# Kernel optimization log

Measured on AMD Instinct MI355X. Metric: run time of the kernel, lower is better.

The kernel has to match this reference:

```python
import jax, jax.numpy as jnp
import numpy as np

N_NODES = 100000
N_EDGES = 1600000
N_FEAT = 64
HIDDEN = 64
OUT = 1
NUM_GRAPHS = 256
N_STACK_LAYERS = 4  # layers 0..3 are 64->64->64; layer 4 is 64->1->1


def setup_inputs() -> dict:
    key = jax.random.key(0)
    ks = jax.random.split(key, 12)
    x = jax.random.normal(ks[0], (N_NODES, N_FEAT), dtype=jnp.float32)
    edge_index = jax.random.randint(ks[1], (2, N_EDGES), 0, N_NODES, dtype=jnp.int64)
    batch = jnp.sort(jax.random.randint(ks[2], (N_NODES,), 0, NUM_GRAPHS, dtype=jnp.int64))
    s = 1.0 / np.sqrt(HIDDEN)
    # Stacked params for the 4 identical (64->64->64) GIN MLPs
    W1 = jax.random.uniform(ks[3], (N_STACK_LAYERS, HIDDEN, HIDDEN), jnp.float32, -s, s)
    b1 = jax.random.uniform(ks[4], (N_STACK_LAYERS, HIDDEN), jnp.float32, -s, s)
    W2 = jax.random.uniform(ks[5], (N_STACK_LAYERS, HIDDEN, HIDDEN), jnp.float32, -s, s)
    b2 = jax.random.uniform(ks[6], (N_STACK_LAYERS, HIDDEN), jnp.float32, -s, s)
    # Last layer MLP: [64 -> 1 -> 1]
    W1_last = jax.random.uniform(ks[7], (HIDDEN, OUT), jnp.float32, -s, s)
    b1_last = jax.random.uniform(ks[8], (OUT,), jnp.float32, -s, s)
    W2_last = jax.random.uniform(ks[9], (OUT, OUT), jnp.float32, -1.0, 1.0)
    b2_last = jax.random.uniform(ks[10], (OUT,), jnp.float32, -1.0, 1.0)
    return {"x": x, "edge_index": edge_index, "batch": batch,
            "W1": W1, "b1": b1, "W2": W2, "b2": b2,
            "W1_last": W1_last, "b1_last": b1_last,
            "W2_last": W2_last, "b2_last": b2_last}


def _gin_conv(x, src, dst, w1, bb1, w2, bb2):
    # GINConv: mlp((1+eps)*x + sum_{j in N(i)} x_j), eps=0
    agg = jax.ops.segment_sum(x[src], dst, num_segments=N_NODES)
    h = agg + x
    h = jnp.maximum(h @ w1 + bb1, 0.0)  # Linear + ReLU inside MLP
    return h @ w2 + bb2                 # plain last Linear of MLP


def reference(x, edge_index, batch, W1, b1, W2, b2, W1_last, b1_last, W2_last, b2_last):
    src, dst = edge_index[0], edge_index[1]  # message: x[src] -> dst (source_to_target)
    h = x
    for i in range(N_STACK_LAYERS):
        h = _gin_conv(h, src, dst, W1[i], b1[i], W2[i], b2[i])
        h = jnp.maximum(h, 0.0)  # inter-layer ReLU (dropout = identity in eval)
    h = _gin_conv(h, src, dst, W1_last, b1_last, W2_last, b2_last)  # last layer: no act
    # global mean pool over graphs
    sums = jax.ops.segment_sum(h, batch, num_segments=NUM_GRAPHS)
    counts = jax.ops.segment_sum(jnp.ones((N_NODES, 1), dtype=h.dtype), batch,
                                 num_segments=NUM_GRAPHS)
    return sums / jnp.maximum(counts, 1.0)
```

## Files before the change

kernel.cpp:

```cpp
#include <hip/hip_runtime.h>
#include <hip/hip_bf16.h>

#define N_NODES 100000
#define N_EDGES 1600000
#define FEAT 64
#define NGRAPH 256

#define SCAN_CHUNK 1024
#define SCAN_BLOCKS ((N_NODES + SCAN_CHUNK - 1) / SCAN_CHUNK)

#define CB_SHIFT 10
#define CB_NODES 1024
#define NCB ((N_NODES + CB_NODES - 1) / CB_NODES)
#define CB_CAP 18432

#define PB 512
#define EPB ((N_EDGES + PB - 1) / PB)

#define NTILES (N_NODES / 16)
#define MLP_BLOCKS 1024

typedef unsigned short u16;
typedef unsigned int u32;
typedef __attribute__((ext_vector_type(8))) short short8;
typedef __attribute__((ext_vector_type(4))) float f32x4;

static __device__ __forceinline__ float bf2f(u16 h) {
    return __uint_as_float(((u32)h) << 16);
}
static __device__ __forceinline__ u16 f2bf(float x) {
    u32 u = __float_as_uint(x);
    return (u16)((u + 0x7FFF + ((u >> 16) & 1)) >> 16);
}
static __device__ __forceinline__ float2 up2(u32 v) {
    return make_float2(bf2f((u16)(v & 0xFFFF)), bf2f((u16)(v >> 16)));
}
static __device__ __forceinline__ short8 as_short8(uint4 v) {
    union { uint4 u; short8 s; } c; c.u = v; return c.s;
}


__global__ __launch_bounds__(256) void k_phist(const int* __restrict__ dst,
                                               int* __restrict__ bhist) {
    __shared__ int cnt[NCB];
    int t = threadIdx.x;
    for (int i = t; i < NCB; i += 256) cnt[i] = 0;
    __syncthreads();
    int begin = blockIdx.x * EPB;
    int end = begin + EPB; if (end > N_EDGES) end = N_EDGES;
    for (int e = begin + t; e < end; e += 256)
        atomicAdd(&cnt[dst[e] >> CB_SHIFT], 1);
    __syncthreads();
    for (int i = t; i < NCB; i += 256) bhist[i * PB + blockIdx.x] = cnt[i];
}

__global__ __launch_bounds__(PB) void k_pscan(int* __restrict__ bhist,
                                              int* __restrict__ gtot) {
    __shared__ int s[PB];
    int b = blockIdx.x, t = threadIdx.x;
    int v = bhist[b * PB + t];
    s[t] = v;
    __syncthreads();
    for (int off = 1; off < PB; off <<= 1) {
        int add = (t >= off) ? s[t - off] : 0;
        __syncthreads();
        s[t] += add;
        __syncthreads();
    }
    int incl = s[t];
    bhist[b * PB + t] = (t ? s[t - 1] : 0);
    if (t == PB - 1) gtot[b] = incl;
}

__global__ __launch_bounds__(256) void k_pscatter(const int* __restrict__ src,
                                                  const int* __restrict__ dst,
                                                  const int* __restrict__ bhist,
                                                  int* __restrict__ tmp) {
    __shared__ int cur[NCB];
    int t = threadIdx.x;
    for (int i = t; i < NCB; i += 256) cur[i] = bhist[i * PB + blockIdx.x];
    __syncthreads();
    int begin = blockIdx.x * EPB;
    int end = begin + EPB; if (end > N_EDGES) end = N_EDGES;
    for (int e = begin + t; e < end; e += 256) {
        int d = dst[e];
        int b = d >> CB_SHIFT;
        int pos = atomicAdd(&cur[b], 1);
        if (pos < CB_CAP) tmp[b * CB_CAP + pos] = ((d & (CB_NODES - 1)) << 17) | src[e];
    }
}


__global__ __launch_bounds__(256) void k_bdeg(const int* __restrict__ tmp,
                                              const int* __restrict__ gtot,
                                              int* __restrict__ deg) {
    __shared__ int cnt[CB_NODES];
    int b = blockIdx.x, t = threadIdx.x;
    for (int j = t; j < CB_NODES; j += 256) cnt[j] = 0;
    __syncthreads();
    int n = gtot[b]; if (n > CB_CAP) n = CB_CAP;
    const int* tp = &tmp[b * CB_CAP];
    for (int i = t; i < n; i += 256) atomicAdd(&cnt[tp[i] >> 17], 1);
    __syncthreads();
    int n0 = b << CB_SHIFT;
    for (int j = t; j < CB_NODES; j += 256) {
        int node = n0 + j;
        if (node < N_NODES) deg[node] = cnt[j];
    }
}


__global__ __launch_bounds__(256) void k_scan1(const int* __restrict__ deg,
                                               int* __restrict__ bsum) {
    int t = threadIdx.x;
    int base = blockIdx.x * SCAN_CHUNK + t * 4;
    int4 d = make_int4(0, 0, 0, 0);
    if (base + 3 < N_NODES) {
        d = *reinterpret_cast<const int4*>(&deg[base]);
    } else {
        if (base + 0 < N_NODES) d.x = deg[base + 0];
        if (base + 1 < N_NODES) d.y = deg[base + 1];
        if (base + 2 < N_NODES) d.z = deg[base + 2];
    }
    int v = d.x + d.y + d.z + d.w;
#pragma unroll
    for (int off = 32; off; off >>= 1) v += __shfl_xor(v, off);
    __shared__ int red[4];
    int lane = t & 63, wid = t >> 6;
    if (lane == 0) red[wid] = v;
    __syncthreads();
    if (t == 0) bsum[blockIdx.x] = red[0] + red[1] + red[2] + red[3];
}

__global__ __launch_bounds__(128) void k_scan2(int* __restrict__ bsum) {
    __shared__ int s[128];
    int t = threadIdx.x;
    int v = (t < SCAN_BLOCKS) ? bsum[t] : 0;
    s[t] = v;
    __syncthreads();
    for (int off = 1; off < 128; off <<= 1) {
        int add = (t >= off) ? s[t - off] : 0;
        __syncthreads();
        s[t] += add;
        __syncthreads();
    }
    if (t < SCAN_BLOCKS) bsum[t] = (t ? s[t - 1] : 0);
}

__global__ __launch_bounds__(256) void k_scan3(int* __restrict__ deg_off,
                                               const int* __restrict__ bsum) {
    int t = threadIdx.x;
    int base = blockIdx.x * SCAN_CHUNK + t * 4;
    int4 d = make_int4(0, 0, 0, 0);
    bool full = (base + 3 < N_NODES);
    if (full) {
        d = *reinterpret_cast<const int4*>(&deg_off[base]);
    } else {
        if (base + 0 < N_NODES) d.x = deg_off[base + 0];
        if (base + 1 < N_NODES) d.y = deg_off[base + 1];
        if (base + 2 < N_NODES) d.z = deg_off[base + 2];
    }
    int total = d.x + d.y + d.z + d.w;
    __shared__ int sc[256];
    sc[t] = total;
    __syncthreads();
    for (int off = 1; off < 256; off <<= 1) {
        int add = (t >= off) ? sc[t - off] : 0;
        __syncthreads();
        sc[t] += add;
        __syncthreads();
    }
    int texc = (t ? sc[t - 1] : 0) + bsum[blockIdx.x];
    int4 o;
    o.x = texc;
    o.y = o.x + d.x;
    o.z = o.y + d.y;
    o.w = o.z + d.z;
    if (full) {
        *reinterpret_cast<int4*>(&deg_off[base]) = o;
    } else {
        if (base + 0 < N_NODES) deg_off[base + 0] = o.x;
        if (base + 1 < N_NODES) deg_off[base + 1] = o.y;
        if (base + 2 < N_NODES) deg_off[base + 2] = o.z;
    }
}


__global__ __launch_bounds__(256) void k_bsort(const int* __restrict__ tmp,
                                               const int* __restrict__ offs,
                                               const int* __restrict__ gtot,
                                               int* __restrict__ ssrc) {
    __shared__ int lcur[CB_NODES];
    int b = blockIdx.x;
    int n0 = b << CB_SHIFT;
    int t = threadIdx.x;
    for (int j = t; j < CB_NODES; j += 256) {
        int n = n0 + j;
        lcur[j] = (n < N_NODES) ? offs[n] : 0;
    }
    __syncthreads();
    int cnt = gtot[b]; if (cnt > CB_CAP) cnt = CB_CAP;
    const int* tp = &tmp[b * CB_CAP];
    for (int i = t; i < cnt; i += 256) {
        int p = tp[i];
        int pos = atomicAdd(&lcur[p >> 17], 1);
        ssrc[pos] = p & 0x1FFFF;
    }
}


__global__ __launch_bounds__(256) void k_cvt(const float* __restrict__ x,
                                             u16* __restrict__ hb) {
    int i = blockIdx.x * 256 + threadIdx.x;
    const int total = N_NODES * FEAT / 8;
    if (i < total) {
        const float4* xv = (const float4*)x;
        float4 a = xv[2 * i], b = xv[2 * i + 1];
        uint4 o;
        o.x = f2bf(a.x) | ((u32)f2bf(a.y) << 16);
        o.y = f2bf(a.z) | ((u32)f2bf(a.w) << 16);
        o.z = f2bf(b.x) | ((u32)f2bf(b.y) << 16);
        o.w = f2bf(b.z) | ((u32)f2bf(b.w) << 16);
        ((uint4*)hb)[i] = o;
    }
}


__global__ __launch_bounds__(256) void k_aggregate(const u16* __restrict__ hb,
                                                   u32* __restrict__ aggb,
                                                   const int* __restrict__ offs,
                                                   const int* __restrict__ ssrc) {
    int grp = threadIdx.x >> 4;
    int li = threadIdx.x & 15;
    int node = blockIdx.x * 16 + grp;
    if (node >= N_NODES) return;
    const uint2* hb2 = (const uint2*)hb;
    uint2 pv = hb2[(size_t)node * 16 + li];
    float2 pa = up2(pv.x), pb = up2(pv.y);
    float v0 = pa.x, v1 = pa.y, v2 = pb.x, v3 = pb.y;
    int s = offs[node];
    int e = (node + 1 < N_NODES) ? offs[node + 1] : N_EDGES;
    int j = s;
    for (; j + 7 < e; j += 8) {
        int s0 = ssrc[j], s1 = ssrc[j + 1], s2 = ssrc[j + 2], s3 = ssrc[j + 3];
        int s4 = ssrc[j + 4], s5 = ssrc[j + 5], s6 = ssrc[j + 6], s7 = ssrc[j + 7];
        uint2 n0 = hb2[(size_t)s0 * 16 + li];
        uint2 n1 = hb2[(size_t)s1 * 16 + li];
        uint2 n2 = hb2[(size_t)s2 * 16 + li];
        uint2 n3 = hb2[(size_t)s3 * 16 + li];
        uint2 n4 = hb2[(size_t)s4 * 16 + li];
        uint2 n5 = hb2[(size_t)s5 * 16 + li];
        uint2 n6 = hb2[(size_t)s6 * 16 + li];
        uint2 n7 = hb2[(size_t)s7 * 16 + li];
        float2 a0 = up2(n0.x), b0 = up2(n0.y), a1 = up2(n1.x), b1 = up2(n1.y);
        float2 a2 = up2(n2.x), b2 = up2(n2.y), a3 = up2(n3.x), b3 = up2(n3.y);
        float2 a4 = up2(n4.x), b4 = up2(n4.y), a5 = up2(n5.x), b5 = up2(n5.y);
        float2 a6 = up2(n6.x), b6 = up2(n6.y), a7 = up2(n7.x), b7 = up2(n7.y);
        v0 += a0.x + a1.x + a2.x + a3.x + a4.x + a5.x + a6.x + a7.x;
        v1 += a0.y + a1.y + a2.y + a3.y + a4.y + a5.y + a6.y + a7.y;
        v2 += b0.x + b1.x + b2.x + b3.x + b4.x + b5.x + b6.x + b7.x;
        v3 += b0.y + b1.y + b2.y + b3.y + b4.y + b5.y + b6.y + b7.y;
    }
    if (j + 3 < e) {
        int s0 = ssrc[j], s1 = ssrc[j + 1], s2 = ssrc[j + 2], s3 = ssrc[j + 3];
        uint2 n0 = hb2[(size_t)s0 * 16 + li];
        uint2 n1 = hb2[(size_t)s1 * 16 + li];
        uint2 n2 = hb2[(size_t)s2 * 16 + li];
        uint2 n3 = hb2[(size_t)s3 * 16 + li];
        float2 a0 = up2(n0.x), b0 = up2(n0.y), a1 = up2(n1.x), b1 = up2(n1.y);
        float2 a2 = up2(n2.x), b2 = up2(n2.y), a3 = up2(n3.x), b3 = up2(n3.y);
        v0 += a0.x + a1.x + a2.x + a3.x;
        v1 += a0.y + a1.y + a2.y + a3.y;
        v2 += b0.x + b1.x + b2.x + b3.x;
        v3 += b0.y + b1.y + b2.y + b3.y;
        j += 4;
    }
    for (; j < e; ++j) {
        uint2 nv = hb2[(size_t)ssrc[j] * 16 + li];
        float2 a = up2(nv.x), b = up2(nv.y);
        v0 += a.x; v1 += a.y; v2 += b.x; v3 += b.y;
    }
    uint2 o;
    o.x = f2bf(v0) | ((u32)f2bf(v1) << 16);
    o.y = f2bf(v2) | ((u32)f2bf(v3) << 16);
    ((uint2*)aggb)[(size_t)node * 16 + li] = o;
}


__global__ __launch_bounds__(256) void k_mlp(const u32* __restrict__ aggb,
                                             u32* __restrict__ hout32,
                                             const float* __restrict__ W1,
                                             const float* __restrict__ b1,
                                             const float* __restrict__ W2,
                                             const float* __restrict__ b2) {
    __shared__ __align__(16) u32 lds[4 * 2 * 576];
    int wid = threadIdx.x >> 6;
    int lane = threadIdx.x & 63;
    int m = lane & 15;
    int g = lane >> 4;
    u32* H = &lds[wid * 2 * 576];
    u32* O = H + 576;

    short8 A1[4][2], A2[4][2];
    float bv1[4][4], bv2[4][4];
#pragma unroll
    for (int nt = 0; nt < 4; ++nt) {
        int n = nt * 16 + m;
#pragma unroll
        for (int kh = 0; kh < 2; ++kh) {
            short8 s1, s2;
#pragma unroll
            for (int j = 0; j < 8; ++j) {
                int k = kh * 32 + g * 8 + j;
                s1[j] = (short)f2bf(W1[k * 64 + n]);
                s2[j] = (short)f2bf(W2[k * 64 + n]);
            }
            A1[nt][kh] = s1;
            A2[nt][kh] = s2;
        }
#pragma unroll
        for (int r = 0; r < 4; ++r) {
            bv1[nt][r] = b1[nt * 16 + g * 4 + r];
            bv2[nt][r] = b2[nt * 16 + g * 4 + r];
        }
    }

    int gwave = blockIdx.x * 4 + wid;
    int nwaves = gridDim.x * 4;
    for (int tile = gwave; tile < NTILES; tile += nwaves) {
        int nodeBase = tile * 16;
        const uint4* bp = (const uint4*)(aggb + (size_t)(nodeBase + m) * 32);
        short8 B0 = as_short8(bp[g]);
        short8 B1f = as_short8(bp[4 + g]);

#pragma unroll
        for (int nt = 0; nt < 4; ++nt) {
            f32x4 acc = { bv1[nt][0], bv1[nt][1], bv1[nt][2], bv1[nt][3] };
            acc = __builtin_amdgcn_mfma_f32_16x16x32_bf16(A1[nt][0], B0, acc, 0, 0, 0);
            acc = __builtin_amdgcn_mfma_f32_16x16x32_bf16(A1[nt][1], B1f, acc, 0, 0, 0);
            float h0 = fmaxf(acc[0], 0.0f), h1 = fmaxf(acc[1], 0.0f);
            float h2 = fmaxf(acc[2], 0.0f), h3 = fmaxf(acc[3], 0.0f);
            H[m * 36 + nt * 8 + g * 2 + 0] = f2bf(h0) | ((u32)f2bf(h1) << 16);
            H[m * 36 + nt * 8 + g * 2 + 1] = f2bf(h2) | ((u32)f2bf(h3) << 16);
        }
        const uint4* hp = (const uint4*)H;
        short8 HB0 = as_short8(hp[9 * m + g]);
        short8 HB1 = as_short8(hp[9 * m + g + 4]);

#pragma unroll
        for (int nt = 0; nt < 4; ++nt) {
            f32x4 acc = { bv2[nt][0], bv2[nt][1], bv2[nt][2], bv2[nt][3] };
            acc = __builtin_amdgcn_mfma_f32_16x16x32_bf16(A2[nt][0], HB0, acc, 0, 0, 0);
            acc = __builtin_amdgcn_mfma_f32_16x16x32_bf16(A2[nt][1], HB1, acc, 0, 0, 0);
            float o0 = fmaxf(acc[0], 0.0f), o1 = fmaxf(acc[1], 0.0f);
            float o2 = fmaxf(acc[2], 0.0f), o3 = fmaxf(acc[3], 0.0f);
            O[m * 36 + nt * 8 + g * 2 + 0] = f2bf(o0) | ((u32)f2bf(o1) << 16);
            O[m * 36 + nt * 8 + g * 2 + 1] = f2bf(o2) | ((u32)f2bf(o3) << 16);
        }
        int m2 = lane >> 2;
        int q = (lane & 3) * 8;
        const uint4* op = (const uint4*)O;
        uint4 w0 = op[(m2 * 36 + q) >> 2];
        uint4 w1 = op[(m2 * 36 + q + 4) >> 2];
        uint4* gp = (uint4*)(hout32 + (size_t)(nodeBase + m2) * 32 + q);
        gp[0] = w0;
        gp[1] = w1;
    }
}


__global__ __launch_bounds__(256) void k_lastagg(const u16* __restrict__ hb,
                                                 const int* __restrict__ offs,
                                                 const int* __restrict__ ssrc,
                                                 const float* __restrict__ W1l,
                                                 const float* __restrict__ b1l,
                                                 const float* __restrict__ W2l,
                                                 const float* __restrict__ b2l,
                                                 float* __restrict__ o) {
    int grp = threadIdx.x >> 4;
    int li = threadIdx.x & 15;
    int node = blockIdx.x * 16 + grp;
    if (node >= N_NODES) return;
    const uint2* hb2 = (const uint2*)hb;
    uint2 pv = hb2[(size_t)node * 16 + li];
    float2 pa = up2(pv.x), pb = up2(pv.y);
    float v0 = pa.x, v1 = pa.y, v2 = pb.x, v3 = pb.y;
    int s = offs[node];
    int e = (node + 1 < N_NODES) ? offs[node + 1] : N_EDGES;
    int j = s;
    for (; j + 7 < e; j += 8) {
        int s0 = ssrc[j], s1 = ssrc[j + 1], s2 = ssrc[j + 2], s3 = ssrc[j + 3];
        int s4 = ssrc[j + 4], s5 = ssrc[j + 5], s6 = ssrc[j + 6], s7 = ssrc[j + 7];
        uint2 n0 = hb2[(size_t)s0 * 16 + li];
        uint2 n1 = hb2[(size_t)s1 * 16 + li];
        uint2 n2 = hb2[(size_t)s2 * 16 + li];
        uint2 n3 = hb2[(size_t)s3 * 16 + li];
        uint2 n4 = hb2[(size_t)s4 * 16 + li];
        uint2 n5 = hb2[(size_t)s5 * 16 + li];
        uint2 n6 = hb2[(size_t)s6 * 16 + li];
        uint2 n7 = hb2[(size_t)s7 * 16 + li];
        float2 a0 = up2(n0.x), b0 = up2(n0.y), a1 = up2(n1.x), b1 = up2(n1.y);
        float2 a2 = up2(n2.x), b2 = up2(n2.y), a3 = up2(n3.x), b3 = up2(n3.y);
        float2 a4 = up2(n4.x), b4 = up2(n4.y), a5 = up2(n5.x), b5 = up2(n5.y);
        float2 a6 = up2(n6.x), b6 = up2(n6.y), a7 = up2(n7.x), b7 = up2(n7.y);
        v0 += a0.x + a1.x + a2.x + a3.x + a4.x + a5.x + a6.x + a7.x;
        v1 += a0.y + a1.y + a2.y + a3.y + a4.y + a5.y + a6.y + a7.y;
        v2 += b0.x + b1.x + b2.x + b3.x + b4.x + b5.x + b6.x + b7.x;
        v3 += b0.y + b1.y + b2.y + b3.y + b4.y + b5.y + b6.y + b7.y;
    }
    if (j + 3 < e) {
        int s0 = ssrc[j], s1 = ssrc[j + 1], s2 = ssrc[j + 2], s3 = ssrc[j + 3];
        uint2 n0 = hb2[(size_t)s0 * 16 + li];
        uint2 n1 = hb2[(size_t)s1 * 16 + li];
        uint2 n2 = hb2[(size_t)s2 * 16 + li];
        uint2 n3 = hb2[(size_t)s3 * 16 + li];
        float2 a0 = up2(n0.x), b0 = up2(n0.y), a1 = up2(n1.x), b1 = up2(n1.y);
        float2 a2 = up2(n2.x), b2 = up2(n2.y), a3 = up2(n3.x), b3 = up2(n3.y);
        v0 += a0.x + a1.x + a2.x + a3.x;
        v1 += a0.y + a1.y + a2.y + a3.y;
        v2 += b0.x + b1.x + b2.x + b3.x;
        v3 += b0.y + b1.y + b2.y + b3.y;
        j += 4;
    }
    for (; j < e; ++j) {
        uint2 nv = hb2[(size_t)ssrc[j] * 16 + li];
        float2 a = up2(nv.x), b = up2(nv.y);
        v0 += a.x; v1 += a.y; v2 += b.x; v3 += b.y;
    }
    float4 wv = ((const float4*)W1l)[li];
    float v = v0 * wv.x + v1 * wv.y + v2 * wv.z + v3 * wv.w;
#pragma unroll
    for (int off = 8; off; off >>= 1) v += __shfl_xor(v, off);
    if (li == 0) {
        float h1 = fmaxf(v + b1l[0], 0.0f);
        o[node] = fmaf(h1, W2l[0], b2l[0]);
    }
}


__global__ __launch_bounds__(256) void k_pool(const float* __restrict__ o,
                                              const int* __restrict__ batch,
                                              float* __restrict__ out) {
    int g = blockIdx.x;
    int lo = 0, hi = N_NODES;
    while (lo < hi) { int mid = (lo + hi) >> 1; if (batch[mid] < g) lo = mid + 1; else hi = mid; }
    int start = lo;
    hi = N_NODES;
    while (lo < hi) { int mid = (lo + hi) >> 1; if (batch[mid] < g + 1) lo = mid + 1; else hi = mid; }
    int end = lo;

    float s = 0.0f;
    for (int i = start + threadIdx.x; i < end; i += 256) s += o[i];
#pragma unroll
    for (int off = 32; off; off >>= 1) s += __shfl_xor(s, off);
    __shared__ float red[4];
    int lane = threadIdx.x & 63, wid = threadIdx.x >> 6;
    if (lane == 0) red[wid] = s;
    __syncthreads();
    if (threadIdx.x == 0) {
        float t = red[0] + red[1] + red[2] + red[3];
        float c = (float)(end - start);
        out[g] = t / fmaxf(c, 1.0f);
    }
}


extern "C" void kernel_launch(void* const* d_in, const int* in_sizes, int n_in,
                              void* d_out, int out_size, void* d_ws, size_t ws_size,
                              hipStream_t stream) {
    const float* x    = (const float*)d_in[0];
    const int*   ei   = (const int*)d_in[1];
    const int*   bat  = (const int*)d_in[2];
    const float* W1   = (const float*)d_in[3];
    const float* b1   = (const float*)d_in[4];
    const float* W2   = (const float*)d_in[5];
    const float* b2   = (const float*)d_in[6];
    const float* W1l  = (const float*)d_in[7];
    const float* b1l  = (const float*)d_in[8];
    const float* W2l  = (const float*)d_in[9];
    const float* b2l  = (const float*)d_in[10];
    float* out = (float*)d_out;

    const int* srcI = ei;
    const int* dstI = ei + N_EDGES;

    char* ws = (char*)d_ws;
    u32*   aggb  = (u32*)ws;                                ws += (size_t)N_NODES * 32 * 4;
    u16*   hb    = (u16*)ws;                                ws += (size_t)N_NODES * FEAT * 2;
    int*   offs  = (int*)ws;                                ws += (size_t)N_NODES * 4;
    int*   ssrc  = (int*)ws;                                ws += (size_t)N_EDGES * 4;
    int*   tmp   = (int*)ws;                                ws += (size_t)NCB * CB_CAP * 4;
    float* onode = (float*)ws;                              ws += (size_t)N_NODES * 4;
    int*   bsum  = (int*)ws;                                ws += 128 * 4;
    int*   bhist = (int*)ws;                                ws += (size_t)NCB * PB * 4;
    int*   gtot  = (int*)ws;                                ws += ((NCB + 3) & ~3) * 4;

    k_phist<<<PB, 256, 0, stream>>>(dstI, bhist);
    k_pscan<<<NCB, PB, 0, stream>>>(bhist, gtot);
    k_pscatter<<<PB, 256, 0, stream>>>(srcI, dstI, bhist, tmp);
    k_bdeg<<<NCB, 256, 0, stream>>>(tmp, gtot, offs);
    k_scan1<<<SCAN_BLOCKS, 256, 0, stream>>>(offs, bsum);
    k_scan2<<<1, 128, 0, stream>>>(bsum);
    k_scan3<<<SCAN_BLOCKS, 256, 0, stream>>>(offs, bsum);
    k_bsort<<<NCB, 256, 0, stream>>>(tmp, offs, gtot, ssrc);
    k_cvt<<<(N_NODES * FEAT / 8 + 255) / 256, 256, 0, stream>>>(x, hb);

    const int ngrid = (N_NODES + 15) / 16;

    for (int l = 0; l < 4; ++l) {
        k_aggregate<<<ngrid, 256, 0, stream>>>(hb, aggb, offs, ssrc);
        k_mlp<<<MLP_BLOCKS, 256, 0, stream>>>(aggb, (u32*)hb,
                                              W1 + (size_t)l * FEAT * FEAT,
                                              b1 + (size_t)l * FEAT,
                                              W2 + (size_t)l * FEAT * FEAT,
                                              b2 + (size_t)l * FEAT);
    }
    k_lastagg<<<ngrid, 256, 0, stream>>>(hb, offs, ssrc, W1l, b1l, W2l, b2l, onode);
    k_pool<<<NGRAPH, 256, 0, stream>>>(onode, bat, out);
}
```

Before: 306.9 us.

## Fuse neighbor aggregation into MLP kernel with ping-pong feature buffers

```diff
diff --git a/kernel.cpp b/kernel.cpp
--- a/kernel.cpp
+++ b/kernel.cpp
@@ -226,80 +226,21 @@
 }
 
 
-__global__ __launch_bounds__(256) void k_aggregate(const u16* __restrict__ hb,
-                                                   u32* __restrict__ aggb,
-                                                   const int* __restrict__ offs,
-                                                   const int* __restrict__ ssrc) {
-    int grp = threadIdx.x >> 4;
-    int li = threadIdx.x & 15;
-    int node = blockIdx.x * 16 + grp;
-    if (node >= N_NODES) return;
-    const uint2* hb2 = (const uint2*)hb;
-    uint2 pv = hb2[(size_t)node * 16 + li];
-    float2 pa = up2(pv.x), pb = up2(pv.y);
-    float v0 = pa.x, v1 = pa.y, v2 = pb.x, v3 = pb.y;
-    int s = offs[node];
-    int e = (node + 1 < N_NODES) ? offs[node + 1] : N_EDGES;
-    int j = s;
-    for (; j + 7 < e; j += 8) {
-        int s0 = ssrc[j], s1 = ssrc[j + 1], s2 = ssrc[j + 2], s3 = ssrc[j + 3];
-        int s4 = ssrc[j + 4], s5 = ssrc[j + 5], s6 = ssrc[j + 6], s7 = ssrc[j + 7];
-        uint2 n0 = hb2[(size_t)s0 * 16 + li];
-        uint2 n1 = hb2[(size_t)s1 * 16 + li];
-        uint2 n2 = hb2[(size_t)s2 * 16 + li];
-        uint2 n3 = hb2[(size_t)s3 * 16 + li];
-        uint2 n4 = hb2[(size_t)s4 * 16 + li];
-        uint2 n5 = hb2[(size_t)s5 * 16 + li];
-        uint2 n6 = hb2[(size_t)s6 * 16 + li];
-        uint2 n7 = hb2[(size_t)s7 * 16 + li];
-        float2 a0 = up2(n0.x), b0 = up2(n0.y), a1 = up2(n1.x), b1 = up2(n1.y);
-        float2 a2 = up2(n2.x), b2 = up2(n2.y), a3 = up2(n3.x), b3 = up2(n3.y);
-        float2 a4 = up2(n4.x), b4 = up2(n4.y), a5 = up2(n5.x), b5 = up2(n5.y);
-        float2 a6 = up2(n6.x), b6 = up2(n6.y), a7 = up2(n7.x), b7 = up2(n7.y);
-        v0 += a0.x + a1.x + a2.x + a3.x + a4.x + a5.x + a6.x + a7.x;
-        v1 += a0.y + a1.y + a2.y + a3.y + a4.y + a5.y + a6.y + a7.y;
-        v2 += b0.x + b1.x + b2.x + b3.x + b4.x + b5.x + b6.x + b7.x;
-        v3 += b0.y + b1.y + b2.y + b3.y + b4.y + b5.y + b6.y + b7.y;
-    }
-    if (j + 3 < e) {
-        int s0 = ssrc[j], s1 = ssrc[j + 1], s2 = ssrc[j + 2], s3 = ssrc[j + 3];
-        uint2 n0 = hb2[(size_t)s0 * 16 + li];
-        uint2 n1 = hb2[(size_t)s1 * 16 + li];
-        uint2 n2 = hb2[(size_t)s2 * 16 + li];
-        uint2 n3 = hb2[(size_t)s3 * 16 + li];
-        float2 a0 = up2(n0.x), b0 = up2(n0.y), a1 = up2(n1.x), b1 = up2(n1.y);
-        float2 a2 = up2(n2.x), b2 = up2(n2.y), a3 = up2(n3.x), b3 = up2(n3.y);
-        v0 += a0.x + a1.x + a2.x + a3.x;
-        v1 += a0.y + a1.y + a2.y + a3.y;
-        v2 += b0.x + b1.x + b2.x + b3.x;
-        v3 += b0.y + b1.y + b2.y + b3.y;
-        j += 4;
-    }
-    for (; j < e; ++j) {
-        uint2 nv = hb2[(size_t)ssrc[j] * 16 + li];
-        float2 a = up2(nv.x), b = up2(nv.y);
-        v0 += a.x; v1 += a.y; v2 += b.x; v3 += b.y;
-    }
-    uint2 o;
-    o.x = f2bf(v0) | ((u32)f2bf(v1) << 16);
-    o.y = f2bf(v2) | ((u32)f2bf(v3) << 16);
-    ((uint2*)aggb)[(size_t)node * 16 + li] = o;
-}
-
-
-__global__ __launch_bounds__(256) void k_mlp(const u32* __restrict__ aggb,
-                                             u32* __restrict__ hout32,
-                                             const float* __restrict__ W1,
-                                             const float* __restrict__ b1,
-                                             const float* __restrict__ W2,
-                                             const float* __restrict__ b2) {
+__global__ __launch_bounds__(256) void k_aggmlp(const u16* __restrict__ hbin,
+                                                u32* __restrict__ hbout32,
+                                                const int* __restrict__ offs,
+                                                const int* __restrict__ ssrc,
+                                                const float* __restrict__ W1,
+                                                const float* __restrict__ b1,
+                                                const float* __restrict__ W2,
+                                                const float* __restrict__ b2) {
     __shared__ __align__(16) u32 lds[4 * 2 * 576];
     int wid = threadIdx.x >> 6;
     int lane = threadIdx.x & 63;
     int m = lane & 15;
     int g = lane >> 4;
-    u32* H = &lds[wid * 2 * 576];
-    u32* O = H + 576;
+    u32* T = &lds[wid * 2 * 576];
+    u32* H = T + 576;
 
     short8 A1[4][2], A2[4][2];
     float bv1[4][4], bv2[4][4];
@@ -325,13 +266,70 @@
         }
     }
 
+    const uint2* hb2 = (const uint2*)hbin;
     int gwave = blockIdx.x * 4 + wid;
     int nwaves = gridDim.x * 4;
     for (int tile = gwave; tile < NTILES; tile += nwaves) {
         int nodeBase = tile * 16;
-        const uint4* bp = (const uint4*)(aggb + (size_t)(nodeBase + m) * 32);
-        short8 B0 = as_short8(bp[g]);
-        short8 B1f = as_short8(bp[4 + g]);
+
+#pragma unroll
+        for (int r = 0; r < 4; ++r) {
+            int nit = r * 4 + g;
+            int node = nodeBase + nit;
+            uint2 pv = hb2[(size_t)node * 16 + m];
+            float2 pa = up2(pv.x), pb = up2(pv.y);
+            float v0 = pa.x, v1 = pa.y, v2 = pb.x, v3 = pb.y;
+            int s = offs[node];
+            int e = (node + 1 < N_NODES) ? offs[node + 1] : N_EDGES;
+            int j = s;
+            for (; j + 7 < e; j += 8) {
+                int s0 = ssrc[j], s1 = ssrc[j + 1], s2 = ssrc[j + 2], s3 = ssrc[j + 3];
+                int s4 = ssrc[j + 4], s5 = ssrc[j + 5], s6 = ssrc[j + 6], s7 = ssrc[j + 7];
+                uint2 n0 = hb2[(size_t)s0 * 16 + m];
+                uint2 n1 = hb2[(size_t)s1 * 16 + m];
+                uint2 n2 = hb2[(size_t)s2 * 16 + m];
+                uint2 n3 = hb2[(size_t)s3 * 16 + m];
+                uint2 n4 = hb2[(size_t)s4 * 16 + m];
+                uint2 n5 = hb2[(size_t)s5 * 16 + m];
+                uint2 n6 = hb2[(size_t)s6 * 16 + m];
+                uint2 n7 = hb2[(size_t)s7 * 16 + m];
+                float2 a0 = up2(n0.x), c0 = up2(n0.y), a1 = up2(n1.x), c1 = up2(n1.y);
+                float2 a2 = up2(n2.x), c2 = up2(n2.y), a3 = up2(n3.x), c3 = up2(n3.y);
+                float2 a4 = up2(n4.x), c4 = up2(n4.y), a5 = up2(n5.x), c5 = up2(n5.y);
+                float2 a6 = up2(n6.x), c6 = up2(n6.y), a7 = up2(n7.x), c7 = up2(n7.y);
+                v0 += a0.x + a1.x + a2.x + a3.x + a4.x + a5.x + a6.x + a7.x;
+                v1 += a0.y + a1.y + a2.y + a3.y + a4.y + a5.y + a6.y + a7.y;
+                v2 += c0.x + c1.x + c2.x + c3.x + c4.x + c5.x + c6.x + c7.x;
+                v3 += c0.y + c1.y + c2.y + c3.y + c4.y + c5.y + c6.y + c7.y;
+            }
+            if (j + 3 < e) {
+                int s0 = ssrc[j], s1 = ssrc[j + 1], s2 = ssrc[j + 2], s3 = ssrc[j + 3];
+                uint2 n0 = hb2[(size_t)s0 * 16 + m];
+                uint2 n1 = hb2[(size_t)s1 * 16 + m];
+                uint2 n2 = hb2[(size_t)s2 * 16 + m];
+                uint2 n3 = hb2[(size_t)s3 * 16 + m];
+                float2 a0 = up2(n0.x), c0 = up2(n0.y), a1 = up2(n1.x), c1 = up2(n1.y);
+                float2 a2 = up2(n2.x), c2 = up2(n2.y), a3 = up2(n3.x), c3 = up2(n3.y);
+                v0 += a0.x + a1.x + a2.x + a3.x;
+                v1 += a0.y + a1.y + a2.y + a3.y;
+                v2 += c0.x + c1.x + c2.x + c3.x;
+                v3 += c0.y + c1.y + c2.y + c3.y;
+                j += 4;
+            }
+            for (; j < e; ++j) {
+                uint2 nv = hb2[(size_t)ssrc[j] * 16 + m];
+                float2 a = up2(nv.x), c = up2(nv.y);
+                v0 += a.x; v1 += a.y; v2 += c.x; v3 += c.y;
+            }
+            uint2 o;
+            o.x = f2bf(v0) | ((u32)f2bf(v1) << 16);
+            o.y = f2bf(v2) | ((u32)f2bf(v3) << 16);
+            *(uint2*)&T[nit * 36 + 2 * m] = o;
+        }
+
+        const uint4* tp4 = (const uint4*)T;
+        short8 B0 = as_short8(tp4[9 * m + g]);
+        short8 B1f = as_short8(tp4[9 * m + 4 + g]);
 
 #pragma unroll
         for (int nt = 0; nt < 4; ++nt) {
@@ -354,15 +352,15 @@
             acc = __builtin_amdgcn_mfma_f32_16x16x32_bf16(A2[nt][1], HB1, acc, 0, 0, 0);
             float o0 = fmaxf(acc[0], 0.0f), o1 = fmaxf(acc[1], 0.0f);
             float o2 = fmaxf(acc[2], 0.0f), o3 = fmaxf(acc[3], 0.0f);
-            O[m * 36 + nt * 8 + g * 2 + 0] = f2bf(o0) | ((u32)f2bf(o1) << 16);
-            O[m * 36 + nt * 8 + g * 2 + 1] = f2bf(o2) | ((u32)f2bf(o3) << 16);
+            T[m * 36 + nt * 8 + g * 2 + 0] = f2bf(o0) | ((u32)f2bf(o1) << 16);
+            T[m * 36 + nt * 8 + g * 2 + 1] = f2bf(o2) | ((u32)f2bf(o3) << 16);
         }
         int m2 = lane >> 2;
         int q = (lane & 3) * 8;
-        const uint4* op = (const uint4*)O;
+        const uint4* op = (const uint4*)T;
         uint4 w0 = op[(m2 * 36 + q) >> 2];
         uint4 w1 = op[(m2 * 36 + q + 4) >> 2];
-        uint4* gp = (uint4*)(hout32 + (size_t)(nodeBase + m2) * 32 + q);
+        uint4* gp = (uint4*)(hbout32 + (size_t)(nodeBase + m2) * 32 + q);
         gp[0] = w0;
         gp[1] = w1;
     }
@@ -485,8 +483,8 @@
     const int* dstI = ei + N_EDGES;
 
     char* ws = (char*)d_ws;
-    u32*   aggb  = (u32*)ws;                                ws += (size_t)N_NODES * 32 * 4;
-    u16*   hb    = (u16*)ws;                                ws += (size_t)N_NODES * FEAT * 2;
+    u16*   hbA   = (u16*)ws;                                ws += (size_t)N_NODES * FEAT * 2;
+    u16*   hbB   = (u16*)ws;                                ws += (size_t)N_NODES * FEAT * 2;
     int*   offs  = (int*)ws;                                ws += (size_t)N_NODES * 4;
     int*   ssrc  = (int*)ws;                                ws += (size_t)N_EDGES * 4;
     int*   tmp   = (int*)ws;                                ws += (size_t)NCB * CB_CAP * 4;
@@ -503,18 +501,19 @@
     k_scan2<<<1, 128, 0, stream>>>(bsum);
     k_scan3<<<SCAN_BLOCKS, 256, 0, stream>>>(offs, bsum);
     k_bsort<<<NCB, 256, 0, stream>>>(tmp, offs, gtot, ssrc);
-    k_cvt<<<(N_NODES * FEAT / 8 + 255) / 256, 256, 0, stream>>>(x, hb);
-
+    k_cvt<<<(N_NODES * FEAT / 8 + 255) / 256, 256, 0, stream>>>(x, hbA);
+
+    const u16* cur = hbA;
+    u16* nxt = hbB;
+    for (int l = 0; l < 4; ++l) {
+        k_aggmlp<<<MLP_BLOCKS, 256, 0, stream>>>(cur, (u32*)nxt, offs, ssrc,
+                                                 W1 + (size_t)l * FEAT * FEAT,
+                                                 b1 + (size_t)l * FEAT,
+                                                 W2 + (size_t)l * FEAT * FEAT,
+                                                 b2 + (size_t)l * FEAT);
+        const u16* t = cur; cur = nxt; nxt = (u16*)t;
+    }
     const int ngrid = (N_NODES + 15) / 16;
-
-    for (int l = 0; l < 4; ++l) {
-        k_aggregate<<<ngrid, 256, 0, stream>>>(hb, aggb, offs, ssrc);
-        k_mlp<<<MLP_BLOCKS, 256, 0, stream>>>(aggb, (u32*)hb,
-                                              W1 + (size_t)l * FEAT * FEAT,
-                                              b1 + (size_t)l * FEAT,
-                                              W2 + (size_t)l * FEAT * FEAT,
-                                              b2 + (size_t)l * FEAT);
-    }
-    k_lastagg<<<ngrid, 256, 0, stream>>>(hb, offs, ssrc, W1l, b1l, W2l, b2l, onode);
+    k_lastagg<<<ngrid, 256, 0, stream>>>(cur, offs, ssrc, W1l, b1l, W2l, b2l, onode);
     k_pool<<<NGRAPH, 256, 0, stream>>>(onode, bat, out);
 }
```

Measured after the change: 370.5 us. 1.21x slower.
